# Performance work log

Hardware: AMD Instinct MI355X
Metric: run time of the kernel (lower is better)

The kernel has to match this reference:

```python
import jax, jax.numpy as jnp
import numpy as np

B, C, K, L, V = 1024, 1024, 20, 2048, 80


def setup_inputs() -> dict:
    key = jax.random.key(0)
    k1, k2, k3, k4, k5 = jax.random.split(key, 5)
    x = jax.random.normal(k1, (B, C), dtype=jnp.float32)
    # small init so exp(linear) stays numerically tame, as in trained models
    W = jax.random.normal(k2, (C, 3 * K), dtype=jnp.float32) * 0.01
    b = jnp.zeros((3 * K,), dtype=jnp.float32)
    kappa_old = jax.random.uniform(k3, (B, K), dtype=jnp.float32) * 5.0
    chars = jax.random.randint(k4, (B, L), 0, V)
    onehots = jax.nn.one_hot(chars, V, dtype=jnp.float32)  # [B, L, V]
    text_lens = jax.random.randint(k5, (B, 1), 1, L + 1).astype(jnp.int32)
    return {"x": x, "W": W, "b": b, "kappa_old": kappa_old,
            "onehots": onehots, "text_lens": text_lens}


def reference(x, W, b, kappa_old, onehots, text_lens):
    Lp = onehots.shape[1]  # padded_text_len
    params = jnp.exp(x @ W + b)                      # [B, 3K]
    alpha, beta, pre_kappa = jnp.split(params, 3, axis=-1)  # each [B, K]
    kappa = kappa_old + pre_kappa                    # [B, K]
    idx = jnp.arange(Lp + 1, dtype=x.dtype)          # [L+1]
    # gravity: [B, K, L+1]
    gravity = -beta[:, :, None] * (kappa[:, :, None] - idx) ** 2
    # phi: sum over K mixture components, then length rescale -> [B, L+1]
    phi = jnp.einsum('bk,bkl->bl', alpha, jnp.exp(gravity))
    phi = phi * (Lp / text_lens.astype(x.dtype))
    # soft window over the one-hot text -> [B, V]
    w = jnp.einsum('bl,blv->bv', phi[:, :Lp], onehots)
    return (w, kappa, phi)
```

## Files before the change

kernel.cpp:

```cpp
#include <hip/hip_runtime.h>

constexpr int B = 1024;
constexpr int C = 1024;
constexpr int K = 20;
constexpr int L = 2048;
constexpr int V = 80;
constexpr int TK = 3 * K;


__global__ __launch_bounds__(256)
void window_fused_kernel(const float* __restrict__ x,
                         const float* __restrict__ W,
                         const float* __restrict__ bias,
                         const float* __restrict__ kappa_old,
                         const float* __restrict__ onehots,
                         const int*   __restrict__ text_lens,
                         float* __restrict__ out) {
    const int b = blockIdx.x;
    const int t = threadIdx.x;

    __shared__ float lds_x[C];
    __shared__ float lds_phi[L + 1];
    __shared__ float lds_abk[TK];
    __shared__ float lds_w[V];

    const float4* oh = reinterpret_cast<const float4*>(onehots + (size_t)b * L * V);

    float4 bufA0 = oh[t];        float4 bufA1 = oh[t + 256];
    float4 bufA2 = oh[t + 512];  float4 bufA3 = oh[t + 768];
    float4 bufB0 = oh[t + 1024]; float4 bufB1 = oh[t + 1280];
    float4 bufB2 = oh[t + 1536]; float4 bufB3 = oh[t + 1792];

    reinterpret_cast<float4*>(lds_x)[t] =
        reinterpret_cast<const float4*>(x + (size_t)b * C)[t];
    if (t < V) lds_w[t] = 0.0f;
    __syncthreads();

    {
        const int g   = t >> 2;
        const int sub = t & 3;
        float acc = 0.0f;
        if (g < TK) {
            const float* Wg = W + g;
            #pragma unroll 8
            for (int i = 0; i < C / 4; ++i) {
                const int c = sub + 4 * i;
                acc += lds_x[c] * Wg[c * TK];
            }
        }
        acc += __shfl_xor(acc, 1);
        acc += __shfl_xor(acc, 2);
        if (sub == 0 && g < TK) {
            const float p = __expf(acc + bias[g]);
            if (g >= 2 * K) {
                const int k = g - 2 * K;
                const float kap = kappa_old[(size_t)b * K + k] + p;
                lds_abk[g] = kap;
                out[(size_t)B * V + (size_t)b * K + k] = kap;
            } else {
                lds_abk[g] = p;
            }
        }
    }
    __syncthreads();

    {
        float s[8];
        #pragma unroll
        for (int j = 0; j < 8; ++j) s[j] = 0.0f;
        #pragma unroll
        for (int k = 0; k < K; ++k) {
            const float a  = lds_abk[k];
            const float be = lds_abk[K + k];
            const float kp = lds_abk[2 * K + k];
            #pragma unroll
            for (int j = 0; j < 8; ++j) {
                const float d = kp - (float)(t + (j << 8));
                s[j] += a * __expf(-be * d * d);
            }
        }
        const float scale = 2048.0f / (float)text_lens[b];
        float* out_phi = out + (size_t)B * V + (size_t)B * K + (size_t)b * (L + 1);
        #pragma unroll
        for (int j = 0; j < 8; ++j) {
            const int l = t + (j << 8);
            const float v = s[j] * scale;
            lds_phi[l] = v;
            out_phi[l] = v;
        }
        if (t == 0) {
            float sv = 0.0f;
            #pragma unroll
            for (int k = 0; k < K; ++k) {
                const float d = lds_abk[2 * K + k] - 2048.0f;
                sv += lds_abk[k] * __expf(-lds_abk[K + k] * d * d);
            }
            out_phi[L] = sv * scale;
        }
    }
    __syncthreads();

    {
        #define PROC(vv, ii) {                                        \
            const int i_ = (ii);                                      \
            const float ph = lds_phi[i_ / 20];                        \
            const int v0 = (i_ % 20) * 4;                             \
            if (vv.x != 0.0f) atomicAdd(&lds_w[v0 + 0], ph * vv.x);   \
            if (vv.y != 0.0f) atomicAdd(&lds_w[v0 + 1], ph * vv.y);   \
            if (vv.z != 0.0f) atomicAdd(&lds_w[v0 + 2], ph * vv.z);   \
            if (vv.w != 0.0f) atomicAdd(&lds_w[v0 + 3], ph * vv.w); }

        #pragma unroll 1
        for (int batch = 0; batch < 40; batch += 2) {
            const int ia = t + (batch << 10);
            PROC(bufA0, ia);       PROC(bufA1, ia + 256);
            PROC(bufA2, ia + 512); PROC(bufA3, ia + 768);
            if (batch + 2 < 40) {
                const int na = t + ((batch + 2) << 10);
                bufA0 = oh[na];        bufA1 = oh[na + 256];
                bufA2 = oh[na + 512];  bufA3 = oh[na + 768];
            }
            const int ib = ia + 1024;
            PROC(bufB0, ib);       PROC(bufB1, ib + 256);
            PROC(bufB2, ib + 512); PROC(bufB3, ib + 768);
            if (batch + 3 < 40) {
                const int nb = t + ((batch + 3) << 10);
                bufB0 = oh[nb];        bufB1 = oh[nb + 256];
                bufB2 = oh[nb + 512];  bufB3 = oh[nb + 768];
            }
        }
        #undef PROC
    }
    __syncthreads();

    if (t < V) out[(size_t)b * V + t] = lds_w[t];
}

extern "C" void kernel_launch(void* const* d_in, const int* in_sizes, int n_in,
                              void* d_out, int out_size, void* d_ws, size_t ws_size,
                              hipStream_t stream) {
    const float* x         = (const float*)d_in[0];
    const float* W         = (const float*)d_in[1];
    const float* bias      = (const float*)d_in[2];
    const float* kappa_old = (const float*)d_in[3];
    const float* onehots   = (const float*)d_in[4];
    const int*   text_lens = (const int*)d_in[5];
    float* out = (float*)d_out;

    window_fused_kernel<<<B, 256, 0, stream>>>(x, W, bias, kappa_old,
                                               onehots, text_lens, out);
}
```

Measured before the change: 159.3 us.

## Split into params/phi kernel and a separate 512-thread one-hot streaming kernel

Splits the fused kernel in two. The first computes the projection, kappa and phi and writes phi to global memory. The second reads phi back into LDS and streams the 671 MB one-hot tensor with 512-thread blocks, using launch bounds that request higher occupancy. The streaming kernel also collapses each float4 into a single LDS atomic by summing the lanes and decoding the active lane index. This assumes strict one-hot inputs and adds a second launch plus a phi round trip through global memory.

Result: slower. 162.6 us (+2.1%).

```diff
diff --git a/kernel.cpp b/kernel.cpp
--- a/kernel.cpp
+++ b/kernel.cpp
@@ -7,33 +7,24 @@
 constexpr int V = 80;
 constexpr int TK = 3 * K;
 
+constexpr size_t OUT_KAPPA = (size_t)B * V;
+constexpr size_t OUT_PHI   = OUT_KAPPA + (size_t)B * K;
 
 __global__ __launch_bounds__(256)
-void window_fused_kernel(const float* __restrict__ x,
-                         const float* __restrict__ W,
-                         const float* __restrict__ bias,
-                         const float* __restrict__ kappa_old,
-                         const float* __restrict__ onehots,
-                         const int*   __restrict__ text_lens,
-                         float* __restrict__ out) {
+void params_phi_kernel(const float* __restrict__ x,
+                       const float* __restrict__ W,
+                       const float* __restrict__ bias,
+                       const float* __restrict__ kappa_old,
+                       const int*   __restrict__ text_lens,
+                       float* __restrict__ out) {
     const int b = blockIdx.x;
     const int t = threadIdx.x;
 
     __shared__ float lds_x[C];
-    __shared__ float lds_phi[L + 1];
     __shared__ float lds_abk[TK];
-    __shared__ float lds_w[V];
-
-    const float4* oh = reinterpret_cast<const float4*>(onehots + (size_t)b * L * V);
-
-    float4 bufA0 = oh[t];        float4 bufA1 = oh[t + 256];
-    float4 bufA2 = oh[t + 512];  float4 bufA3 = oh[t + 768];
-    float4 bufB0 = oh[t + 1024]; float4 bufB1 = oh[t + 1280];
-    float4 bufB2 = oh[t + 1536]; float4 bufB3 = oh[t + 1792];
 
     reinterpret_cast<float4*>(lds_x)[t] =
         reinterpret_cast<const float4*>(x + (size_t)b * C)[t];
-    if (t < V) lds_w[t] = 0.0f;
     __syncthreads();
 
     {
@@ -56,7 +47,7 @@
                 const int k = g - 2 * K;
                 const float kap = kappa_old[(size_t)b * K + k] + p;
                 lds_abk[g] = kap;
-                out[(size_t)B * V + (size_t)b * K + k] = kap;
+                out[OUT_KAPPA + (size_t)b * K + k] = kap;
             } else {
                 lds_abk[g] = p;
             }
@@ -80,14 +71,10 @@
             }
         }
         const float scale = 2048.0f / (float)text_lens[b];
-        float* out_phi = out + (size_t)B * V + (size_t)B * K + (size_t)b * (L + 1);
+        float* out_phi = out + OUT_PHI + (size_t)b * (L + 1);
         #pragma unroll
-        for (int j = 0; j < 8; ++j) {
-            const int l = t + (j << 8);
-            const float v = s[j] * scale;
-            lds_phi[l] = v;
-            out_phi[l] = v;
-        }
+        for (int j = 0; j < 8; ++j)
+            out_phi[t + (j << 8)] = s[j] * scale;
         if (t == 0) {
             float sv = 0.0f;
             #pragma unroll
@@ -98,41 +85,65 @@
             out_phi[L] = sv * scale;
         }
     }
+}
+
+__global__ __launch_bounds__(512, 6)
+void window_stream_kernel(const float* __restrict__ onehots,
+                          float* __restrict__ out) {
+    const int b = blockIdx.x;
+    const int t = threadIdx.x;
+
+    __shared__ float lds_phi[L];
+    __shared__ float lds_w[V];
+
+    {
+        const float* phi_src = out + OUT_PHI + (size_t)b * (L + 1);
+        #pragma unroll
+        for (int i = 0; i < L / 512; ++i)
+            lds_phi[t + i * 512] = phi_src[t + i * 512];
+    }
+    if (t < V) lds_w[t] = 0.0f;
     __syncthreads();
 
-    {
-        #define PROC(vv, ii) {                                        \
-            const int i_ = (ii);                                      \
-            const float ph = lds_phi[i_ / 20];                        \
-            const int v0 = (i_ % 20) * 4;                             \
-            if (vv.x != 0.0f) atomicAdd(&lds_w[v0 + 0], ph * vv.x);   \
-            if (vv.y != 0.0f) atomicAdd(&lds_w[v0 + 1], ph * vv.y);   \
-            if (vv.z != 0.0f) atomicAdd(&lds_w[v0 + 2], ph * vv.z);   \
-            if (vv.w != 0.0f) atomicAdd(&lds_w[v0 + 3], ph * vv.w); }
+    const float4* oh = reinterpret_cast<const float4*>(onehots + (size_t)b * L * V);
 
-        #pragma unroll 1
-        for (int batch = 0; batch < 40; batch += 2) {
-            const int ia = t + (batch << 10);
-            PROC(bufA0, ia);       PROC(bufA1, ia + 256);
-            PROC(bufA2, ia + 512); PROC(bufA3, ia + 768);
-            if (batch + 2 < 40) {
-                const int na = t + ((batch + 2) << 10);
-                bufA0 = oh[na];        bufA1 = oh[na + 256];
-                bufA2 = oh[na + 512];  bufA3 = oh[na + 768];
-            }
-            const int ib = ia + 1024;
-            PROC(bufB0, ib);       PROC(bufB1, ib + 256);
-            PROC(bufB2, ib + 512); PROC(bufB3, ib + 768);
-            if (batch + 3 < 40) {
-                const int nb = t + ((batch + 3) << 10);
-                bufB0 = oh[nb];        bufB1 = oh[nb + 256];
-                bufB2 = oh[nb + 512];  bufB3 = oh[nb + 768];
-            }
+    #define PROC(vv, jj) {                                                  \
+        const float s_ = vv.x + vv.y + vv.z + vv.w;                         \
+        if (s_ != 0.0f) {                                                   \
+            const int i_ = t + (jj) * 512;                                  \
+            const float ph = lds_phi[i_ / 20];                              \
+            const int v0 = (i_ % 20) * 4;                                   \
+            const int jo = (int)(vv.y + 2.0f * vv.z + 3.0f * vv.w);         \
+            atomicAdd(&lds_w[v0 + jo], ph * s_);                            \
+        } }
+
+    float4 a0 = oh[t];            float4 a1 = oh[t + 512];
+    float4 a2 = oh[t + 1024];     float4 a3 = oh[t + 1536];
+    float4 b0 = oh[t + 2048];     float4 b1 = oh[t + 2560];
+    float4 b2 = oh[t + 3072];     float4 b3 = oh[t + 3584];
+
+    #pragma unroll 1
+    for (int q = 0; q < 20; q += 2) {
+        const int ja = q * 4;
+        PROC(a0, ja);     PROC(a1, ja + 1);
+        PROC(a2, ja + 2); PROC(a3, ja + 3);
+        if (q + 2 < 20) {
+            const int na = t + (q + 2) * 2048;
+            a0 = oh[na];        a1 = oh[na + 512];
+            a2 = oh[na + 1024]; a3 = oh[na + 1536];
         }
-        #undef PROC
+        const int jb = ja + 4;
+        PROC(b0, jb);     PROC(b1, jb + 1);
+        PROC(b2, jb + 2); PROC(b3, jb + 3);
+        if (q + 3 < 20) {
+            const int nb = t + (q + 3) * 2048;
+            b0 = oh[nb];        b1 = oh[nb + 512];
+            b2 = oh[nb + 1024]; b3 = oh[nb + 1536];
+        }
     }
+    #undef PROC
+
     __syncthreads();
-
     if (t < V) out[(size_t)b * V + t] = lds_w[t];
 }
 
@@ -147,6 +158,6 @@
     const int*   text_lens = (const int*)d_in[5];
     float* out = (float*)d_out;
 
-    window_fused_kernel<<<B, 256, 0, stream>>>(x, W, bias, kappa_old,
-                                               onehots, text_lens, out);
+    params_phi_kernel<<<B, 256, 0, stream>>>(x, W, bias, kappa_old, text_lens, out);
+    window_stream_kernel<<<B, 512, 0, stream>>>(onehots, out);
 }
```
